# Kernel tuning notes

Measured on AMD Instinct MI355X. Metric: run time of the kernel, lower is better.

## Reference

```python
import jax, jax.numpy as jnp
import numpy as np

VEC_SIZE = 128
N_VECS = 8
N_ROWS = 256  # n_choices * redundancy
BATCH = 512
EPS = 1e-8


def _combos(n):
    # combos[i, j] = 0 if bit j of i is set else 1  -> shape [2^n, n]
    i = np.arange(2 ** n)[:, None]
    j = np.arange(n)[None, :]
    return jnp.asarray(((i >> j) & 1) == 0, dtype=jnp.float32)


def setup_inputs() -> dict:
    key = jax.random.key(0)
    kq, kw = jax.random.split(key)
    query = jax.random.normal(kq, (BATCH, N_VECS * VEC_SIZE), dtype=jnp.float32)
    weight = jax.random.normal(kw, (N_ROWS, N_VECS * VEC_SIZE), dtype=jnp.float32)
    # match torch init: weight rows normalized over full flattened dim
    weight = weight / jnp.clip(jnp.linalg.norm(weight, axis=1, keepdims=True), EPS)
    return {"query": query, "weight": weight}


def reference(query, weight):
    combos = _combos(N_VECS)                               # [C, n]  C = 2^n
    q = query.reshape(-1, N_VECS, VEC_SIZE)                # [b, n, v]
    w = weight.reshape(-1, N_VECS, VEC_SIZE)               # [r, n, v]
    # cosine similarity over vec_size, per (batch row, weight row, vec slot)
    dot = jnp.einsum('bnv,rnv->brn', q, w)                 # [b, r, n]
    qn = jnp.maximum(jnp.linalg.norm(q, axis=-1), EPS)     # [b, n]
    wn = jnp.maximum(jnp.linalg.norm(w, axis=-1), EPS)     # [r, n]
    cos_sim = dot / (qn[:, None, :] * wn[None, :, :])
    cos_sim = jax.nn.relu(cos_sim)                         # [b, r, n]
    # NAND combo interpolation then product over the n_vecs axis
    cs = cos_sim[:, :, None, :]                            # [b, r, 1, n]
    c = combos[None, None, :, :]                           # [1, 1, C, n]
    transformed = c * cs + (1.0 - c) * (1.0 - cs)          # [b, r, C, n]
    return jnp.prod(transformed, axis=-1)                  # [b, r, C]
```

## Files before the change

kernel.cpp:

```cpp
#include <hip/hip_runtime.h>
#include <math.h>

#define BATCH  512
#define NROWS  256
#define NVECS  8
#define VSIZE  128
#define DIM    1024
#define NCOMBO 256

__global__ __launch_bounds__(256) void fused_kernel(
    const float* __restrict__ q, const float* __restrict__ w,
    float* __restrict__ out) {
  __shared__ __align__(16) float Ws[8 * 1056];
  __shared__ __align__(16) float Cs[8 * 64];
  const int t    = threadIdx.x;
  const int wv   = t >> 6, lane = t & 63;
  const int bs   = blockIdx.x * 8, rs = blockIdx.y * 8;
  const int n    = lane >> 3, c = lane & 7;
  const int koff = n * VSIZE + c * 16;
  const int b0   = bs + 2 * wv;

  #pragma unroll
  for (int i = 0; i < 8; ++i) {
    int f = i * 256 + t;
    int g = f << 2;
    int row = g >> 10, e = g & 1023;
    float4 v = *(const float4*)(w + (size_t)(rs + row) * DIM + e);
    *(float4*)(Ws + row * 1056 + (e >> 7) * 132 + (e & 127)) = v;
  }

  float4 qa[4], qb[4];
  float qs0 = 0.f, qs1 = 0.f;
  {
    const float* Q0 = q + (size_t)b0 * DIM + koff;
    #pragma unroll
    for (int j = 0; j < 4; ++j) {
      qa[j] = *(const float4*)(Q0 + 4 * j);
      qb[j] = *(const float4*)(Q0 + DIM + 4 * j);
      qs0 = fmaf(qa[j].x, qa[j].x, qs0); qs0 = fmaf(qa[j].y, qa[j].y, qs0);
      qs0 = fmaf(qa[j].z, qa[j].z, qs0); qs0 = fmaf(qa[j].w, qa[j].w, qs0);
      qs1 = fmaf(qb[j].x, qb[j].x, qs1); qs1 = fmaf(qb[j].y, qb[j].y, qs1);
      qs1 = fmaf(qb[j].z, qb[j].z, qs1); qs1 = fmaf(qb[j].w, qb[j].w, qs1);
    }
  }
  #pragma unroll
  for (int m = 1; m <= 4; m <<= 1) {
    qs0 += __shfl_xor(qs0, m, 64);
    qs1 += __shfl_xor(qs1, m, 64);
  }
  const float iq0 = 1.0f / fmaxf(sqrtf(qs0), 1e-8f);
  const float iq1 = 1.0f / fmaxf(sqrtf(qs1), 1e-8f);

  __syncthreads();

  const float* Wb = Ws + n * 132 + c * 16;
  #pragma unroll 2
  for (int r = 0; r < 8; ++r) {
    const float* Wr = Wb + r * 1056;
    float s0 = 0.f, s1 = 0.f, wss = 0.f;
    #pragma unroll
    for (int j = 0; j < 4; ++j) {
      float4 w4 = *(const float4*)(Wr + 4 * j);
      s0 = fmaf(qa[j].x, w4.x, s0); s0 = fmaf(qa[j].y, w4.y, s0);
      s0 = fmaf(qa[j].z, w4.z, s0); s0 = fmaf(qa[j].w, w4.w, s0);
      s1 = fmaf(qb[j].x, w4.x, s1); s1 = fmaf(qb[j].y, w4.y, s1);
      s1 = fmaf(qb[j].z, w4.z, s1); s1 = fmaf(qb[j].w, w4.w, s1);
      wss = fmaf(w4.x, w4.x, wss); wss = fmaf(w4.y, w4.y, wss);
      wss = fmaf(w4.z, w4.z, wss); wss = fmaf(w4.w, w4.w, wss);
    }
    #pragma unroll
    for (int m = 1; m <= 4; m <<= 1) {
      s0  += __shfl_xor(s0, m, 64);
      s1  += __shfl_xor(s1, m, 64);
      wss += __shfl_xor(wss, m, 64);
    }
    const float iw  = 1.0f / fmaxf(sqrtf(wss), 1e-8f);
    const float cs0 = fmaxf(s0 * iq0 * iw, 0.f);
    const float cs1 = fmaxf(s1 * iq1 * iw, 0.f);
    float csv = (c == 0) ? cs0 : cs1;
    if (c < 2) Cs[(2 * wv + c) * 64 + r * 8 + n] = csv;
  }

  const bool m2 = lane & 1,  m3 = lane & 2,  m4 = lane & 4;
  const bool m5 = lane & 8,  m6 = lane & 16, m7 = lane & 32;
  float* outL = out + lane * 4;
  #pragma unroll 4
  for (int pi = 0; pi < 16; ++pi) {
    const int p = wv * 16 + pi;
    float4 va = *(const float4*)(Cs + p * 8);
    float4 vb = *(const float4*)(Cs + p * 8 + 4);
    float t2 = m2 ? 1.f - va.z : va.z;
    float t3 = m3 ? 1.f - va.w : va.w;
    float t4 = m4 ? 1.f - vb.x : vb.x;
    float t5 = m5 ? 1.f - vb.y : vb.y;
    float t6 = m6 ? 1.f - vb.z : vb.z;
    float t7 = m7 ? 1.f - vb.w : vb.w;
    float base = ((t2 * t3) * (t4 * t5)) * (t6 * t7);
    float c0 = va.x, c1 = va.y;
    float4 o;
    o.x = base * (c0 * c1);
    o.y = base * ((1.f - c0) * c1);
    o.z = base * (c0 * (1.f - c1));
    o.w = base * ((1.f - c0) * (1.f - c1));
    *(float4*)(outL +
        ((size_t)(bs + (p >> 3)) * NROWS + (rs + (p & 7))) * NCOMBO) = o;
  }
}

extern "C" void kernel_launch(void* const* d_in, const int* in_sizes, int n_in,
                              void* d_out, int out_size, void* d_ws, size_t ws_size,
                              hipStream_t stream) {
  const float* query  = (const float*)d_in[0];
  const float* weight = (const float*)d_in[1];
  float* out = (float*)d_out;
  (void)d_ws; (void)ws_size;

  hipLaunchKernelGGL(fused_kernel, dim3(64, 32), dim3(256), 0, stream,
                     query, weight, out);
}
```

Baseline: 145.1 us.

## Split fused kernel into cosine-similarity and combo-expand kernels via workspace

Breaks the single fused kernel into two launches. The first computes the clamped cosine similarities straight from global memory, without the LDS weight staging, and writes them to a workspace buffer. The second kernel expands each similarity vector into the 256 NAND-combo products and streams out the large output. The aim is to decouple the store-bound expansion from the compute phase so each runs at its own occupancy. The cost is an extra launch plus a workspace round trip, and the original fused path remains as a fallback when no workspace is provided.

```diff
diff --git a/kernel.cpp b/kernel.cpp
--- a/kernel.cpp
+++ b/kernel.cpp
@@ -7,6 +7,100 @@
 #define VSIZE  128
 #define DIM    1024
 #define NCOMBO 256
+
+
+__global__ __launch_bounds__(256) void cos_kernel(
+    const float* __restrict__ q, const float* __restrict__ w,
+    float* __restrict__ cs) {
+  const int t    = threadIdx.x;
+  const int wv   = t >> 6, lane = t & 63;
+  const int bs   = blockIdx.x * 8, rs = blockIdx.y * 8;
+  const int c    = lane & 7, n = lane >> 3;
+  const int koff = lane * 16;
+  const int b0   = bs + 2 * wv;
+
+  float4 qa[4], qb[4];
+  float qs0 = 0.f, qs1 = 0.f;
+  {
+    const float* Q0 = q + (size_t)b0 * DIM + koff;
+    #pragma unroll
+    for (int j = 0; j < 4; ++j) {
+      qa[j] = *(const float4*)(Q0 + 4 * j);
+      qb[j] = *(const float4*)(Q0 + DIM + 4 * j);
+      qs0 = fmaf(qa[j].x, qa[j].x, qs0); qs0 = fmaf(qa[j].y, qa[j].y, qs0);
+      qs0 = fmaf(qa[j].z, qa[j].z, qs0); qs0 = fmaf(qa[j].w, qa[j].w, qs0);
+      qs1 = fmaf(qb[j].x, qb[j].x, qs1); qs1 = fmaf(qb[j].y, qb[j].y, qs1);
+      qs1 = fmaf(qb[j].z, qb[j].z, qs1); qs1 = fmaf(qb[j].w, qb[j].w, qs1);
+    }
+  }
+  #pragma unroll
+  for (int m = 1; m <= 4; m <<= 1) {
+    qs0 += __shfl_xor(qs0, m, 64);
+    qs1 += __shfl_xor(qs1, m, 64);
+  }
+  const float iq0 = 1.0f / fmaxf(sqrtf(qs0), 1e-8f);
+  const float iq1 = 1.0f / fmaxf(sqrtf(qs1), 1e-8f);
+
+  #pragma unroll 2
+  for (int r = 0; r < 8; ++r) {
+    const float* Wr = w + (size_t)(rs + r) * DIM + koff;
+    float s0 = 0.f, s1 = 0.f, wss = 0.f;
+    #pragma unroll
+    for (int j = 0; j < 4; ++j) {
+      float4 w4 = *(const float4*)(Wr + 4 * j);
+      s0 = fmaf(qa[j].x, w4.x, s0); s0 = fmaf(qa[j].y, w4.y, s0);
+      s0 = fmaf(qa[j].z, w4.z, s0); s0 = fmaf(qa[j].w, w4.w, s0);
+      s1 = fmaf(qb[j].x, w4.x, s1); s1 = fmaf(qb[j].y, w4.y, s1);
+      s1 = fmaf(qb[j].z, w4.z, s1); s1 = fmaf(qb[j].w, w4.w, s1);
+      wss = fmaf(w4.x, w4.x, wss); wss = fmaf(w4.y, w4.y, wss);
+      wss = fmaf(w4.z, w4.z, wss); wss = fmaf(w4.w, w4.w, wss);
+    }
+    #pragma unroll
+    for (int m = 1; m <= 4; m <<= 1) {
+      s0  += __shfl_xor(s0, m, 64);
+      s1  += __shfl_xor(s1, m, 64);
+      wss += __shfl_xor(wss, m, 64);
+    }
+    const float iw  = 1.0f / fmaxf(sqrtf(wss), 1e-8f);
+    const float cs0 = fmaxf(s0 * iq0 * iw, 0.f);
+    const float cs1 = fmaxf(s1 * iq1 * iw, 0.f);
+    if (c < 2) {
+      float csv = (c == 0) ? cs0 : cs1;
+      cs[((size_t)(b0 + c) * NROWS + (rs + r)) * 8 + n] = csv;
+    }
+  }
+}
+
+__global__ __launch_bounds__(256) void expand_kernel(
+    const float* __restrict__ cs, float* __restrict__ out) {
+  const int t    = threadIdx.x;
+  const int wv   = t >> 6, lane = t & 63;
+  const bool m2 = lane & 1,  m3 = lane & 2,  m4 = lane & 4;
+  const bool m5 = lane & 8,  m6 = lane & 16, m7 = lane & 32;
+  const int wbase = (blockIdx.x * 4 + wv) * 16;
+  float* outL = out + lane * 4;
+  #pragma unroll 4
+  for (int it = 0; it < 16; ++it) {
+    const int p = __builtin_amdgcn_readfirstlane(wbase + it);
+    const float* cp = cs + ((size_t)p << 3);
+    float4 va = *(const float4*)(cp);
+    float4 vb = *(const float4*)(cp + 4);
+    float t2 = m2 ? 1.f - va.z : va.z;
+    float t3 = m3 ? 1.f - va.w : va.w;
+    float t4 = m4 ? 1.f - vb.x : vb.x;
+    float t5 = m5 ? 1.f - vb.y : vb.y;
+    float t6 = m6 ? 1.f - vb.z : vb.z;
+    float t7 = m7 ? 1.f - vb.w : vb.w;
+    float base = ((t2 * t3) * (t4 * t5)) * (t6 * t7);
+    float c0 = va.x, c1 = va.y;
+    float4 o;
+    o.x = base * (c0 * c1);
+    o.y = base * ((1.f - c0) * c1);
+    o.z = base * (c0 * (1.f - c1));
+    o.w = base * ((1.f - c0) * (1.f - c1));
+    *(float4*)(outL + ((size_t)p << 8)) = o;
+  }
+}
 
 __global__ __launch_bounds__(256) void fused_kernel(
     const float* __restrict__ q, const float* __restrict__ w,
@@ -113,8 +207,16 @@
   const float* query  = (const float*)d_in[0];
   const float* weight = (const float*)d_in[1];
   float* out = (float*)d_out;
-  (void)d_ws; (void)ws_size;
-
-  hipLaunchKernelGGL(fused_kernel, dim3(64, 32), dim3(256), 0, stream,
-                     query, weight, out);
-}
+
+  const size_t cs_bytes = (size_t)BATCH * NROWS * NVECS * sizeof(float);
+  if (d_ws != nullptr && ws_size >= cs_bytes) {
+    float* cs = (float*)d_ws;
+    hipLaunchKernelGGL(cos_kernel, dim3(64, 32), dim3(256), 0, stream,
+                       query, weight, cs);
+    hipLaunchKernelGGL(expand_kernel, dim3(2048), dim3(256), 0, stream,
+                       cs, out);
+  } else {
+    hipLaunchKernelGGL(fused_kernel, dim3(64, 32), dim3(256), 0, stream,
+                       query, weight, out);
+  }
+}
```

Result: slower. 159.7 us (+10.1%).
